# Kernel optimization log

Measured on AMD Instinct MI355X. Metric: run time of the kernel, lower is better.

## Reference

```python
import jax, jax.numpy as jnp
import numpy as np

B, S, D = 64, 14, 2048   # batch, enc_image_size, encoder_dim
A, H, E = 512, 512, 512  # attention_dim, lstm_size, embedding_size
V, L = 10000, 20         # vocab_size, max caption length (T = L-1 decode steps)


def setup_inputs() -> dict:
    key = jax.random.key(0)
    ks = jax.random.split(key, 24)
    p = lambda k, shape: jax.random.normal(k, shape, jnp.float32) * 0.02
    features = jax.random.normal(ks[0], (B, S, S, D), jnp.float32)
    captions = jax.random.randint(ks[1], (B, L), 0, V)
    # sorted descending lengths in [2, L], max forced to L so T_dec = L-1
    lengths = jnp.sort(jax.random.randint(ks[2], (B,), 2, L + 1))[::-1]
    lengths = lengths.at[0].set(L)
    return {
        'features': features, 'captions': captions, 'lengths': lengths,
        'emb': p(ks[3], (V, E)),
        'W_ih': p(ks[4], (4 * H, D + E)), 'b_ih': p(ks[5], (4 * H,)),
        'W_hh': p(ks[6], (4 * H, H)), 'b_hh': p(ks[7], (4 * H,)),
        'h_fc_w': p(ks[8], (H, D)), 'h_fc_b': p(ks[9], (H,)),
        'c_fc_w': p(ks[10], (H, D)), 'c_fc_b': p(ks[11], (H,)),
        'f_beta_w': p(ks[12], (D, H)), 'f_beta_b': p(ks[13], (D,)),
        'cls_w': p(ks[14], (V, H)), 'cls_b': p(ks[15], (V,)),
        'enc_w': p(ks[16], (A, D)), 'enc_b': p(ks[17], (A,)),
        'dec_w': p(ks[18], (A, H)), 'dec_b': p(ks[19], (A,)),
        'att_w': p(ks[20], (1, A)), 'att_b': p(ks[21], (1,)),
    }


def reference(features, captions, lengths, emb, W_ih, b_ih, W_hh, b_hh,
              h_fc_w, h_fc_b, c_fc_w, c_fc_b, f_beta_w, f_beta_b,
              cls_w, cls_b, enc_w, enc_b, dec_w, dec_b, att_w, att_b):
    feats = features.reshape(features.shape[0], -1, features.shape[-1])  # (B,P,D)
    emb_seq = emb[captions]                                              # (B,L,E)
    mean_f = feats.mean(axis=1)
    h = mean_f @ h_fc_w.T + h_fc_b
    c = mean_f @ c_fc_w.T + c_fc_b
    dec_len = lengths - 1
    T = captions.shape[1] - 1
    # attention encoder projection is time-invariant: hoist out of the loop
    att1 = jnp.einsum('bpd,ad->bpa', feats, enc_w) + enc_b               # (B,P,A)

    def step(carry, xs):
        h, c = carry
        x_emb, t = xs
        att2 = h @ dec_w.T + dec_b                                       # (B,A)
        e = jnp.einsum('bpa,a->bp', jax.nn.relu(att1 + att2[:, None, :]), att_w[0]) + att_b[0]
        alpha = jax.nn.softmax(e, axis=1)                                # (B,P)
        awe = jnp.einsum('bp,bpd->bd', alpha, feats)
        gate = jax.nn.sigmoid(h @ f_beta_w.T + f_beta_b)
        awe = gate * awe
        x = jnp.concatenate([x_emb, awe], axis=1)                        # (B,E+D)
        gates = x @ W_ih.T + b_ih + h @ W_hh.T + b_hh                    # torch gate order i,f,g,o
        i, f, g, o = jnp.split(gates, 4, axis=1)
        c2 = jax.nn.sigmoid(f) * c + jax.nn.sigmoid(i) * jnp.tanh(g)
        h2 = jax.nn.sigmoid(o) * jnp.tanh(c2)
        y = h2 @ cls_w.T + cls_b                                         # dropout = eval identity
        active = (t < dec_len)[:, None]
        return (h2, c2), (jnp.where(active, y, 0.0), jnp.where(active, alpha, 0.0))

    xs = (jnp.swapaxes(emb_seq[:, :T], 0, 1), jnp.arange(T))
    (_, _), (y_pred, alphas) = jax.lax.scan(step, (h, c), xs)
    return jnp.swapaxes(y_pred, 0, 1), jnp.swapaxes(alphas, 0, 1)
```

## Files before the change

### kernel.cpp

```cpp
#include <hip/hip_runtime.h>
#include <math.h>

typedef __attribute__((ext_vector_type(8))) short bf16x8;
typedef __attribute__((ext_vector_type(8))) unsigned short u16x8;
typedef __attribute__((ext_vector_type(4))) float f32x4;

#define NB 64
#define NP 196
#define ND 2048
#define NA 512
#define NH 512
#define NE 512
#define NV 10000
#define NT 19
#define NROW (NB*NP)
#define NVP 10112
#define MROW 1280
#define NHP 4608

__device__ __forceinline__ unsigned short f2bu(float f){
    unsigned int u; __builtin_memcpy(&u, &f, 4);
    u = (u + 0x7FFFu + ((u >> 16) & 1u)) >> 16;
    return (unsigned short)u;
}
__device__ __forceinline__ float b2f(unsigned short s){
    unsigned int u = ((unsigned int)s) << 16;
    float f; __builtin_memcpy(&f, &u, 4); return f;
}
__device__ __forceinline__ float sigm(float x){ return 1.f/(1.f + __expf(-x)); }

__device__ __forceinline__ void gll16(const void* g, void* l){
    __builtin_amdgcn_global_load_lds(
        (const __attribute__((address_space(1))) void*)g,
        (__attribute__((address_space(3))) void*)l, 16, 0, 0);
}


__global__ void k_prep(const float4* __restrict__ enc_w, const float4* __restrict__ dec_w,
                       const float4* __restrict__ f_beta_w, const float4* __restrict__ W_ih,
                       const float4* __restrict__ W_hh, const float4* __restrict__ h_fc_w,
                       const float4* __restrict__ c_fc_w, const float4* __restrict__ cls_w,
                       ushort4* __restrict__ encwb, ushort4* __restrict__ whp,
                       ushort4* __restrict__ wgates, ushort4* __restrict__ wembb,
                       ushort4* __restrict__ whc, ushort4* __restrict__ clswb,
                       ushort4* __restrict__ hsb_pad){
    const int n0 = NA*ND/4;
    const int n1 = NHP*512/4;
    const int n2 = 2048*2048/4;
    const int n3 = 2048*512/4;
    const int n4 = 1024*2048/4;
    const int n5 = NVP*NH/4;
    const int n6 = 64*512/4;
    const int total = n0+n1+n2+n3+n4+n5+n6;
    int stride = gridDim.x*blockDim.x;
    for (int i = blockIdx.x*blockDim.x + threadIdx.x; i < total; i += stride){
        int idx = i;
        float4 v; ushort4 o;
        if (idx < n0){
            v = enc_w[idx];
            o.x = f2bu(v.x); o.y = f2bu(v.y); o.z = f2bu(v.z); o.w = f2bu(v.w);
            encwb[idx] = o; continue;
        }
        idx -= n0;
        if (idx < n1){
            if (idx < 512*512/4) v = dec_w[idx];
            else if (idx < 2560*512/4) v = f_beta_w[idx - 512*512/4];
            else v = W_hh[idx - 2560*512/4];
            o.x = f2bu(v.x); o.y = f2bu(v.y); o.z = f2bu(v.z); o.w = f2bu(v.w);
            whp[idx] = o; continue;
        }
        idx -= n1;
        if (idx < n2){
            int j = idx >> 9, kk4 = idx & 511;
            v = W_ih[(size_t)j*640 + 128 + kk4];
            o.x = f2bu(v.x); o.y = f2bu(v.y); o.z = f2bu(v.z); o.w = f2bu(v.w);
            wgates[idx] = o; continue;
        }
        idx -= n2;
        if (idx < n3){
            int j = idx >> 7, kk4 = idx & 127;
            v = W_ih[(size_t)j*640 + kk4];
            o.x = f2bu(v.x); o.y = f2bu(v.y); o.z = f2bu(v.z); o.w = f2bu(v.w);
            wembb[idx] = o; continue;
        }
        idx -= n3;
        if (idx < n4){
            v = (idx < 512*2048/4) ? h_fc_w[idx] : c_fc_w[idx - 512*2048/4];
            o.x = f2bu(v.x); o.y = f2bu(v.y); o.z = f2bu(v.z); o.w = f2bu(v.w);
            whc[idx] = o; continue;
        }
        idx -= n4;
        if (idx < n5){
            if (idx < NV*NH/4){
                v = cls_w[idx];
                o.x = f2bu(v.x); o.y = f2bu(v.y); o.z = f2bu(v.z); o.w = f2bu(v.w);
            } else { o.x = 0; o.y = 0; o.z = 0; o.w = 0; }
            clswb[idx] = o; continue;
        }
        idx -= n5;
        o.x = 0; o.y = 0; o.z = 0; o.w = 0;
        hsb_pad[idx] = o;
    }
}

__global__ void k_cm(const float* __restrict__ feats,
                     unsigned short* __restrict__ fbf,
                     unsigned short* __restrict__ meanbf){
    __shared__ float4 msum[256];
    int dc = blockIdx.x;
    int b  = blockIdx.y;
    int tid = threadIdx.x;
    int c4 = tid & 63;
    int rq = tid >> 6;
    int D0 = dc*256;
    float4 acc = {0.f,0.f,0.f,0.f};
    for (int p = rq; p < NP; p += 4){
        float4 v = *(const float4*)(feats + ((size_t)(b*NP + p))*ND + D0 + c4*4);
        acc.x += v.x; acc.y += v.y; acc.z += v.z; acc.w += v.w;
        ushort4 u4;
        u4.x = f2bu(v.x); u4.y = f2bu(v.y); u4.z = f2bu(v.z); u4.w = f2bu(v.w);
        *(ushort4*)(fbf + ((size_t)(b*NP + p))*ND + D0 + c4*4) = u4;
    }
    msum[tid] = acc;
    __syncthreads();
    if (tid < 64){
        float4 s0 = msum[tid], s1 = msum[tid+64], s2 = msum[tid+128], s3 = msum[tid+192];
        float4 tot = { (s0.x+s1.x)+(s2.x+s3.x), (s0.y+s1.y)+(s2.y+s3.y),
                       (s0.z+s1.z)+(s2.z+s3.z), (s0.w+s1.w)+(s2.w+s3.w) };
        ushort4 o;
        o.x = f2bu(tot.x*(1.f/196.f)); o.y = f2bu(tot.y*(1.f/196.f));
        o.z = f2bu(tot.z*(1.f/196.f)); o.w = f2bu(tot.w*(1.f/196.f));
        *(ushort4*)(meanbf + (size_t)b*ND + D0 + tid*4) = o;
    }
}

__global__ void k_embg(const float* __restrict__ emb, const int* __restrict__ captions,
                       unsigned short* __restrict__ embcat){
    int blk = blockIdx.x, tid = threadIdx.x;
    int r = blk*4 + (tid >> 6);
    int cg = tid & 63;
    u16x8 o;
    #pragma unroll
    for (int k = 0; k < 8; k++) o[k] = 0;
    if (r < NT*64){
        int t = r >> 6, b = r & 63;
        int tok = captions[b*20 + t];
        const float* e = emb + (size_t)tok*NE + cg*8;
        float4 v0 = *(const float4*)e;
        float4 v1 = *(const float4*)(e + 4);
        o[0] = f2bu(v0.x); o[1] = f2bu(v0.y); o[2] = f2bu(v0.z); o[3] = f2bu(v0.w);
        o[4] = f2bu(v1.x); o[5] = f2bu(v1.y); o[6] = f2bu(v1.z); o[7] = f2bu(v1.w);
    }
    *(u16x8*)(embcat + (size_t)r*NE + cg*8) = o;
}

__global__ void k_hc0m(const unsigned short* __restrict__ meanbf,
                       const unsigned short* __restrict__ whc,
                       const float* __restrict__ h_fc_b, const float* __restrict__ c_fc_b,
                       unsigned short* __restrict__ hbf, float* __restrict__ cst){
    int tid = threadIdx.x;
    int w = tid >> 6, l = tid & 63;
    int nt = blockIdx.x;
    int row = 16*w + (l & 15);
    int col = nt*16 + (l & 15);
    int kg = (l >> 4) * 8;
    f32x4 acc = {};
    for (int k0 = 0; k0 < ND; k0 += 32){
        bf16x8 af = *(const bf16x8*)(meanbf + (size_t)row*ND + k0 + kg);
        bf16x8 bv = *(const bf16x8*)(whc + (size_t)col*ND + k0 + kg);
        acc = __builtin_amdgcn_mfma_f32_16x16x32_bf16(af, bv, acc, 0, 0, 0);
    }
    int r0 = 16*w + (l >> 4)*4;
    #pragma unroll
    for (int r = 0; r < 4; r++){
        int b = r0 + r;
        if (col < 512) hbf[b*NH + col] = f2bu(acc[r] + h_fc_b[col]);
        else           cst[b*NH + (col - 512)] = acc[r] + c_fc_b[col - 512];
    }
}

template<int K>
__device__ __forceinline__ void gemm128(const unsigned short* __restrict__ A,
                                        const unsigned short* __restrict__ B,
                                        int brow, int bcol, f32x4 acc[4][4]){
    __shared__ unsigned short As[128*32];
    __shared__ unsigned short Bs[128*32];
    int tid = threadIdx.x;
    int w = tid >> 6, l = tid & 63;
    int wr = (w >> 1) * 64, wc = (w & 1) * 64;
    int lr = l & 15, kg = (l >> 4) * 8;
    const unsigned short* ga0 = A + (size_t)(brow + (tid >> 2))*K + (tid & 3)*8;
    const unsigned short* gb0 = B + (size_t)(bcol + (tid >> 2))*K + (tid & 3)*8;
    for (int k0 = 0; k0 < K; k0 += 32){
        __syncthreads();
        gll16(ga0 + k0,                As + w*512);
        gll16(ga0 + (size_t)64*K + k0, As + 2048 + w*512);
        gll16(gb0 + k0,                Bs + w*512);
        gll16(gb0 + (size_t)64*K + k0, Bs + 2048 + w*512);
        __syncthreads();
        bf16x8 af[4], bfr[4];
        #pragma unroll
        for (int mi = 0; mi < 4; mi++)
            af[mi] = *(const bf16x8*)(As + (wr + mi*16 + lr)*32 + kg);
        #pragma unroll
        for (int ni = 0; ni < 4; ni++)
            bfr[ni] = *(const bf16x8*)(Bs + (wc + ni*16 + lr)*32 + kg);
        #pragma unroll
        for (int ni = 0; ni < 4; ni++){
            #pragma unroll
            for (int mi = 0; mi < 4; mi++)
                acc[mi][ni] = __builtin_amdgcn_mfma_f32_16x16x32_bf16(af[mi], bfr[ni], acc[mi][ni], 0, 0, 0);
        }
    }
}

__global__ void k_gemm_att1(const unsigned short* __restrict__ fbf,
                            const unsigned short* __restrict__ encw,
                            const float* __restrict__ enc_b,
                            unsigned short* __restrict__ att1){
    f32x4 acc[4][4] = {};
    int brow = blockIdx.x*128, bcol = blockIdx.y*128;
    gemm128<ND>(fbf, encw, brow, bcol, acc);
    int w = threadIdx.x >> 6, l = threadIdx.x & 63;
    int wr = (w >> 1) * 64, wc = (w & 1) * 64;
    int r0 = brow + wr + (l >> 4)*4;
    int c0 = bcol + wc + (l & 15);
    #pragma unroll
    for (int ni = 0; ni < 4; ni++){
        int col = c0 + ni*16;
        float eb = enc_b[col];
        #pragma unroll
        for (int mi = 0; mi < 4; mi++){
            #pragma unroll
            for (int r = 0; r < 4; r++)
                att1[(size_t)(r0 + mi*16 + r)*NA + col] = f2bu(acc[mi][ni][r] + eb);
        }
    }
}

__global__ void k_gemb(const unsigned short* __restrict__ embcat,
                       const unsigned short* __restrict__ wembb,
                       const float* __restrict__ b_ih, const float* __restrict__ b_hh,
                       float* __restrict__ gemb){
    f32x4 acc[4][4] = {};
    int brow = blockIdx.x*128, bcol = blockIdx.y*128;
    gemm128<NE>(embcat, wembb, brow, bcol, acc);
    int w = threadIdx.x >> 6, l = threadIdx.x & 63;
    int wr = (w >> 1) * 64, wc = (w & 1) * 64;
    int r0 = brow + wr + (l >> 4)*4;
    int c0 = bcol + wc + (l & 15);
    #pragma unroll
    for (int ni = 0; ni < 4; ni++){
        int col = c0 + ni*16;
        float bias = b_ih[col] + b_hh[col];
        #pragma unroll
        for (int mi = 0; mi < 4; mi++){
            #pragma unroll
            for (int r = 0; r < 4; r++)
                gemb[(size_t)(r0 + mi*16 + r)*2048 + col] = acc[mi][ni][r] + bias;
        }
    }
}

__global__ void k_gemm_cls(const unsigned short* __restrict__ hsb,
                           const unsigned short* __restrict__ clsw,
                           const float* __restrict__ cls_b,
                           const int* __restrict__ lengths,
                           float* __restrict__ yout){
    f32x4 acc[4][4] = {};
    int brow = blockIdx.x*128, bcol = blockIdx.y*128;
    gemm128<NH>(hsb, clsw, brow, bcol, acc);
    int w = threadIdx.x >> 6, l = threadIdx.x & 63;
    int wr = (w >> 1) * 64, wc = (w & 1) * 64;
    int r0 = brow + wr + (l >> 4)*4;
    int c0 = bcol + wc + (l & 15);
    #pragma unroll
    for (int ni = 0; ni < 4; ni++){
        int col = c0 + ni*16;
        if (col >= NV) continue;
        float cb = cls_b[col];
        #pragma unroll
        for (int mi = 0; mi < 4; mi++){
            #pragma unroll
            for (int r = 0; r < 4; r++){
                int grow = r0 + mi*16 + r;
                if (grow >= NT*64) continue;
                int t = grow >> 6, bb = grow & 63;
                int active = t < (lengths[bb] - 1);
                yout[((size_t)bb*NT + t)*NV + col] = active ? (acc[mi][ni][r] + cb) : 0.f;
            }
        }
    }
}


__global__ void k_lstm(const float* __restrict__ part, const float* __restrict__ gemb,
                       const float* __restrict__ hp,
                       float* __restrict__ cst, unsigned short* __restrict__ hbf,
                       unsigned short* __restrict__ hsb, int t){
    int idx = blockIdx.x*256 + threadIdx.x;
    int b = idx >> 9, j = idx & 511;
    const float* ge = gemb + ((size_t)(t - 1)*64 + b)*2048;
    const float* hh = hp + (size_t)b*NHP + 2560;
    float gi = ge[j]        + hh[j];
    float gf = ge[512 + j]  + hh[512 + j];
    float gg = ge[1024 + j] + hh[1024 + j];
    float go = ge[1536 + j] + hh[1536 + j];
    #pragma unroll
    for (int s = 0; s < 8; s++){
        const float* pb = part + (size_t)(s*64 + b)*2048;
        gi += pb[j]; gf += pb[512 + j]; gg += pb[1024 + j]; go += pb[1536 + j];
    }
    float c = cst[b*NH + j];
    float c2 = sigm(gf)*c + sigm(gi)*tanhf(gg);
    float h2 = sigm(go)*tanhf(c2);
    cst[b*NH + j] = c2;
    unsigned short u = f2bu(h2);
    hbf[b*NH + j] = u;
    hsb[((size_t)(t - 1)*64 + b)*NH + j] = u;
}

__global__ void k_hall(const unsigned short* __restrict__ hbf,
                       const unsigned short* __restrict__ whp,
                       const float* __restrict__ dec_b, const float* __restrict__ f_beta_b,
                       float* __restrict__ hp){
    int w = threadIdx.x >> 6, l = threadIdx.x & 63;
    int nt = blockIdx.x;
    int row = 16*w + (l & 15);
    int col = nt*16 + (l & 15);
    int kg = (l >> 4) * 8;
    f32x4 acc = {};
    for (int k0 = 0; k0 < NH; k0 += 32){
        bf16x8 af = *(const bf16x8*)(hbf + row*NH + k0 + kg);
        bf16x8 bv = *(const bf16x8*)(whp + (size_t)col*NH + k0 + kg);
        acc = __builtin_amdgcn_mfma_f32_16x16x32_bf16(af, bv, acc, 0, 0, 0);
    }
    int r0 = 16*w + (l >> 4)*4;
    float bias = (col < 512) ? dec_b[col] : ((col < 2560) ? f_beta_b[col - 512] : 0.f);
    #pragma unroll
    for (int r = 0; r < 4; r++)
        hp[(size_t)(r0 + r)*NHP + col] = acc[r] + bias;
}

__global__ void k_e(const unsigned short* __restrict__ att1,
                    const float* __restrict__ hp,
                    const float* __restrict__ att_w, const float* __restrict__ att_b,
                    float* __restrict__ ews){
    __shared__ float at2[NA];
    __shared__ float aw[NA];
    int b = blockIdx.x >> 2, pc = blockIdx.x & 3;
    int tid = threadIdx.x;
    for (int j = tid; j < NA; j += 256){
        at2[j] = hp[(size_t)b*NHP + j];
        aw[j]  = att_w[j];
    }
    __syncthreads();
    int pl = tid >> 2, q = tid & 3;
    if (pl < 49){
        int p = pc*49 + pl;
        const unsigned short* arow = att1 + ((size_t)(b*NP + p))*NA + q*128;
        float s = 0.f;
        for (int a0 = 0; a0 < 128; a0 += 8){
            bf16x8 v = *(const bf16x8*)(arow + a0);
            #pragma unroll
            for (int e = 0; e < 8; e++){
                int ai = q*128 + a0 + e;
                float x = b2f((unsigned short)v[e]) + at2[ai];
                s += fmaxf(x, 0.f) * aw[ai];
            }
        }
        s += __shfl_xor(s, 1);
        s += __shfl_xor(s, 2);
        if (q == 0) ews[b*NP + p] = s + att_b[0];
    }
}

__global__ void k_awe(const float* __restrict__ ews, const unsigned short* __restrict__ fbf,
                      const float* __restrict__ hp, const int* __restrict__ lengths,
                      unsigned short* __restrict__ xg, float* __restrict__ alphas, int t){
    __shared__ float al[NP];
    __shared__ float red[256];
    int dc = blockIdx.x;
    int b  = blockIdx.y;
    int tid = threadIdx.x;
    float v = (tid < NP) ? ews[b*NP + tid] : -1e30f;
    red[tid] = v; __syncthreads();
    for (int s = 128; s > 0; s >>= 1){ if (tid < s) red[tid] = fmaxf(red[tid], red[tid+s]); __syncthreads(); }
    float m = red[0]; __syncthreads();
    float ev = (tid < NP) ? __expf(v - m) : 0.f;
    red[tid] = ev; __syncthreads();
    for (int s = 128; s > 0; s >>= 1){ if (tid < s) red[tid] += red[tid+s]; __syncthreads(); }
    float inv = 1.f / red[0];
    if (tid < NP) al[tid] = ev * inv;
    __syncthreads();
    if (dc == 0 && tid < NP){
        int active = t < (lengths[b] - 1);
        alphas[((size_t)b*NT + t)*NP + tid] = active ? al[tid] : 0.f;
    }
    int d = dc*256 + tid;
    const unsigned short* fb = fbf + (size_t)(b*NP)*ND + d;
    float a0 = 0.f, a1 = 0.f, a2 = 0.f, a3 = 0.f;
    for (int p = 0; p < 196; p += 4){
        a0 += al[p]     * b2f(fb[(size_t)p*ND]);
        a1 += al[p + 1] * b2f(fb[(size_t)(p + 1)*ND]);
        a2 += al[p + 2] * b2f(fb[(size_t)(p + 2)*ND]);
        a3 += al[p + 3] * b2f(fb[(size_t)(p + 3)*ND]);
    }
    float accv = (a0 + a1) + (a2 + a3);
    float g = sigm(hp[(size_t)b*NHP + 512 + d]);
    xg[b*2048 + d] = f2bu(g * accv);
}

__global__ void k_gates(const unsigned short* __restrict__ xg,
                        const unsigned short* __restrict__ wgates,
                        float* __restrict__ part){
    int nt = blockIdx.x;
    int s  = blockIdx.y;
    int w = threadIdx.x >> 6, l = threadIdx.x & 63;
    int row = 16*w + (l & 15);
    int col = nt*16 + (l & 15);
    int kg = (l >> 4) * 8;
    const unsigned short* arow = xg + row*2048 + s*256;
    const unsigned short* brow = wgates + (size_t)col*2048 + s*256;
    f32x4 acc = {};
    for (int k0 = 0; k0 < 256; k0 += 32){
        bf16x8 af = *(const bf16x8*)(arow + k0 + kg);
        bf16x8 bv = *(const bf16x8*)(brow + k0 + kg);
        acc = __builtin_amdgcn_mfma_f32_16x16x32_bf16(af, bv, acc, 0, 0, 0);
    }
    int r0 = 16*w + (l >> 4)*4;
    #pragma unroll
    for (int r = 0; r < 4; r++)
        part[(size_t)(s*64 + r0 + r)*2048 + col] = acc[r];
}

__global__ void k_lstm_fin(const float* __restrict__ part, const float* __restrict__ gemb,
                           const float* __restrict__ hp,
                           const float* __restrict__ cst, unsigned short* __restrict__ hsb){
    int idx = blockIdx.x*256 + threadIdx.x;
    int b = idx >> 9, j = idx & 511;
    const float* ge = gemb + ((size_t)(NT - 1)*64 + b)*2048;
    const float* hh = hp + (size_t)b*NHP + 2560;
    float gi = ge[j]        + hh[j];
    float gf = ge[512 + j]  + hh[512 + j];
    float gg = ge[1024 + j] + hh[1024 + j];
    float go = ge[1536 + j] + hh[1536 + j];
    #pragma unroll
    for (int s = 0; s < 8; s++){
        const float* pb = part + (size_t)(s*64 + b)*2048;
        gi += pb[j]; gf += pb[512 + j]; gg += pb[1024 + j]; go += pb[1536 + j];
    }
    float c = cst[b*NH + j];
    float c2 = sigm(gf)*c + sigm(gi)*tanhf(gg);
    float h2 = sigm(go)*tanhf(c2);
    hsb[((size_t)(NT - 1)*64 + b)*NH + j] = f2bu(h2);
}


extern "C" void kernel_launch(void* const* d_in, const int* in_sizes, int n_in,
                              void* d_out, int out_size, void* d_ws, size_t ws_size,
                              hipStream_t stream){
    const float* features = (const float*)d_in[0];
    const int*   captions = (const int*)d_in[1];
    const int*   lengths  = (const int*)d_in[2];
    const float* emb      = (const float*)d_in[3];
    const float* W_ih     = (const float*)d_in[4];
    const float* b_ih     = (const float*)d_in[5];
    const float* W_hh     = (const float*)d_in[6];
    const float* b_hh     = (const float*)d_in[7];
    const float* h_fc_w   = (const float*)d_in[8];
    const float* h_fc_b   = (const float*)d_in[9];
    const float* c_fc_w   = (const float*)d_in[10];
    const float* c_fc_b   = (const float*)d_in[11];
    const float* f_beta_w = (const float*)d_in[12];
    const float* f_beta_b = (const float*)d_in[13];
    const float* cls_w    = (const float*)d_in[14];
    const float* cls_b    = (const float*)d_in[15];
    const float* enc_w    = (const float*)d_in[16];
    const float* enc_b    = (const float*)d_in[17];
    const float* dec_w    = (const float*)d_in[18];
    const float* dec_b    = (const float*)d_in[19];
    const float* att_w    = (const float*)d_in[20];
    const float* att_b    = (const float*)d_in[21];

    char* w = (char*)d_ws;
    size_t off = 0;
    auto alloc = [&](size_t bytes)->char*{
        char* p = w + off;
        off += (bytes + 255) & ~(size_t)255;
        return p;
    };
    unsigned short* fbf    = (unsigned short*)alloc((size_t)NROW*ND*2);
    unsigned short* att1   = (unsigned short*)alloc((size_t)NROW*NA*2);
    unsigned short* encwb  = (unsigned short*)alloc((size_t)NA*ND*2);
    unsigned short* whp    = (unsigned short*)alloc((size_t)NHP*NH*2);
    unsigned short* wgates = (unsigned short*)alloc((size_t)2048*2048*2);
    unsigned short* wembb  = (unsigned short*)alloc((size_t)2048*NE*2);
    unsigned short* whc    = (unsigned short*)alloc((size_t)1024*ND*2);
    unsigned short* clswb  = (unsigned short*)alloc((size_t)NVP*NH*2);
    unsigned short* embcat = (unsigned short*)alloc((size_t)MROW*NE*2);
    unsigned short* hsb    = (unsigned short*)alloc((size_t)MROW*NH*2);
    unsigned short* hbf    = (unsigned short*)alloc((size_t)64*NH*2);
    unsigned short* xg     = (unsigned short*)alloc((size_t)64*2048*2);
    unsigned short* meanbf = (unsigned short*)alloc((size_t)64*ND*2);
    float* gemb  = (float*)alloc((size_t)MROW*2048*4);
    float* cst   = (float*)alloc((size_t)64*NH*4);
    float* hp    = (float*)alloc((size_t)64*NHP*4);
    float* ews   = (float*)alloc((size_t)64*NP*4);
    float* part  = (float*)alloc((size_t)8*64*2048*4);

    float* yout = (float*)d_out;
    float* alphas_out = yout + (size_t)NB*NT*NV;

    k_cm<<<dim3(8, 64), 256, 0, stream>>>(features, fbf, meanbf);
    k_prep<<<2048, 256, 0, stream>>>((const float4*)enc_w, (const float4*)dec_w,
                                     (const float4*)f_beta_w, (const float4*)W_ih,
                                     (const float4*)W_hh, (const float4*)h_fc_w,
                                     (const float4*)c_fc_w, (const float4*)cls_w,
                                     (ushort4*)encwb, (ushort4*)whp, (ushort4*)wgates,
                                     (ushort4*)wembb, (ushort4*)whc, (ushort4*)clswb,
                                     (ushort4*)(hsb + (size_t)NT*64*NH));
    k_embg<<<320, 256, 0, stream>>>(emb, captions, embcat);
    k_hc0m<<<64, 256, 0, stream>>>(meanbf, whc, h_fc_b, c_fc_b, hbf, cst);
    k_gemm_att1<<<dim3(98, 4), 256, 0, stream>>>(fbf, encwb, enc_b, att1);
    k_gemb<<<dim3(10, 16), 256, 0, stream>>>(embcat, wembb, b_ih, b_hh, gemb);

    for (int t = 0; t < NT; t++){
        if (t > 0)
            k_lstm<<<128, 256, 0, stream>>>(part, gemb, hp, cst, hbf, hsb, t);
        k_hall<<<288, 256, 0, stream>>>(hbf, whp, dec_b, f_beta_b, hp);
        k_e<<<256, 256, 0, stream>>>(att1, hp, att_w, att_b, ews);
        k_awe<<<dim3(8, 64), 256, 0, stream>>>(ews, fbf, hp, lengths, xg, alphas_out, t);
        k_gates<<<dim3(128, 8), 256, 0, stream>>>(xg, wgates, part);
    }
    k_lstm_fin<<<128, 256, 0, stream>>>(part, gemb, hp, cst, hsb);
    k_gemm_cls<<<dim3(10, 79), 256, 0, stream>>>(hsb, clswb, cls_b, lengths, yout);
}
```

Baseline: 1.054 ms.

## Fuse attention score with weighted sum, and gate GEMM with LSTM cell update

The per-step loop drops from five kernels to three. Attention scores and softmax are now computed inside the weighted-sum kernel, with each block redoing the full score pass for its batch row. The gate GEMM now does split-K reduction through shared memory within a 1024-thread block, with an interleaved column layout so one wave holds all four gates and can apply the LSTM cell update directly. This removes the ews and part global round-trips and several launches per step. The cost is redundant score computation (4x per batch row) and fewer blocks (256 and 128), which risks lower parallelism.

```diff
diff --git a/kernel.cpp b/kernel.cpp
--- a/kernel.cpp
+++ b/kernel.cpp
@@ -294,32 +294,6 @@
 }
 
 
-__global__ void k_lstm(const float* __restrict__ part, const float* __restrict__ gemb,
-                       const float* __restrict__ hp,
-                       float* __restrict__ cst, unsigned short* __restrict__ hbf,
-                       unsigned short* __restrict__ hsb, int t){
-    int idx = blockIdx.x*256 + threadIdx.x;
-    int b = idx >> 9, j = idx & 511;
-    const float* ge = gemb + ((size_t)(t - 1)*64 + b)*2048;
-    const float* hh = hp + (size_t)b*NHP + 2560;
-    float gi = ge[j]        + hh[j];
-    float gf = ge[512 + j]  + hh[512 + j];
-    float gg = ge[1024 + j] + hh[1024 + j];
-    float go = ge[1536 + j] + hh[1536 + j];
-    #pragma unroll
-    for (int s = 0; s < 8; s++){
-        const float* pb = part + (size_t)(s*64 + b)*2048;
-        gi += pb[j]; gf += pb[512 + j]; gg += pb[1024 + j]; go += pb[1536 + j];
-    }
-    float c = cst[b*NH + j];
-    float c2 = sigm(gf)*c + sigm(gi)*tanhf(gg);
-    float h2 = sigm(go)*tanhf(c2);
-    cst[b*NH + j] = c2;
-    unsigned short u = f2bu(h2);
-    hbf[b*NH + j] = u;
-    hsb[((size_t)(t - 1)*64 + b)*NH + j] = u;
-}
-
 __global__ void k_hall(const unsigned short* __restrict__ hbf,
                        const unsigned short* __restrict__ whp,
                        const float* __restrict__ dec_b, const float* __restrict__ f_beta_b,
@@ -342,13 +316,18 @@
         hp[(size_t)(r0 + r)*NHP + col] = acc[r] + bias;
 }
 
-__global__ void k_e(const unsigned short* __restrict__ att1,
-                    const float* __restrict__ hp,
-                    const float* __restrict__ att_w, const float* __restrict__ att_b,
-                    float* __restrict__ ews){
+__global__ void k_eawe(const unsigned short* __restrict__ att1,
+                       const float* __restrict__ hp,
+                       const unsigned short* __restrict__ fbf,
+                       const float* __restrict__ att_w, const float* __restrict__ att_b,
+                       const int* __restrict__ lengths,
+                       unsigned short* __restrict__ xg, float* __restrict__ alphas, int t){
     __shared__ float at2[NA];
     __shared__ float aw[NA];
-    int b = blockIdx.x >> 2, pc = blockIdx.x & 3;
+    __shared__ float sc[200];
+    __shared__ float red[256];
+    int dc = blockIdx.x;
+    int b  = blockIdx.y;
     int tid = threadIdx.x;
     for (int j = tid; j < NA; j += 256){
         at2[j] = hp[(size_t)b*NHP + j];
@@ -356,104 +335,114 @@
     }
     __syncthreads();
     int pl = tid >> 2, q = tid & 3;
-    if (pl < 49){
-        int p = pc*49 + pl;
-        const unsigned short* arow = att1 + ((size_t)(b*NP + p))*NA + q*128;
-        float s = 0.f;
-        for (int a0 = 0; a0 < 128; a0 += 8){
-            bf16x8 v = *(const bf16x8*)(arow + a0);
-            #pragma unroll
-            for (int e = 0; e < 8; e++){
-                int ai = q*128 + a0 + e;
-                float x = b2f((unsigned short)v[e]) + at2[ai];
-                s += fmaxf(x, 0.f) * aw[ai];
+    float ab = att_b[0];
+    #pragma unroll
+    for (int pc = 0; pc < 4; pc++){
+        if (pl < 49){
+            int p = pc*49 + pl;
+            const unsigned short* arow = att1 + ((size_t)(b*NP + p))*NA + q*128;
+            float s = 0.f;
+            for (int a0 = 0; a0 < 128; a0 += 8){
+                bf16x8 v = *(const bf16x8*)(arow + a0);
+                #pragma unroll
+                for (int e = 0; e < 8; e++){
+                    int ai = q*128 + a0 + e;
+                    float x = b2f((unsigned short)v[e]) + at2[ai];
+                    s += fmaxf(x, 0.f) * aw[ai];
+                }
             }
-        }
-        s += __shfl_xor(s, 1);
-        s += __shfl_xor(s, 2);
-        if (q == 0) ews[b*NP + p] = s + att_b[0];
-    }
-}
-
-__global__ void k_awe(const float* __restrict__ ews, const unsigned short* __restrict__ fbf,
-                      const float* __restrict__ hp, const int* __restrict__ lengths,
-                      unsigned short* __restrict__ xg, float* __restrict__ alphas, int t){
-    __shared__ float al[NP];
-    __shared__ float red[256];
-    int dc = blockIdx.x;
-    int b  = blockIdx.y;
-    int tid = threadIdx.x;
-    float v = (tid < NP) ? ews[b*NP + tid] : -1e30f;
+            s += __shfl_xor(s, 1);
+            s += __shfl_xor(s, 2);
+            if (q == 0) sc[p] = s + ab;
+        }
+    }
+    __syncthreads();
+    float v = (tid < NP) ? sc[tid] : -1e30f;
     red[tid] = v; __syncthreads();
-    for (int s = 128; s > 0; s >>= 1){ if (tid < s) red[tid] = fmaxf(red[tid], red[tid+s]); __syncthreads(); }
+    for (int st = 128; st > 0; st >>= 1){ if (tid < st) red[tid] = fmaxf(red[tid], red[tid+st]); __syncthreads(); }
     float m = red[0]; __syncthreads();
     float ev = (tid < NP) ? __expf(v - m) : 0.f;
     red[tid] = ev; __syncthreads();
-    for (int s = 128; s > 0; s >>= 1){ if (tid < s) red[tid] += red[tid+s]; __syncthreads(); }
+    for (int st = 128; st > 0; st >>= 1){ if (tid < st) red[tid] += red[tid+st]; __syncthreads(); }
     float inv = 1.f / red[0];
-    if (tid < NP) al[tid] = ev * inv;
+    __syncthreads();
+    if (tid < NP) sc[tid] = ev * inv;
     __syncthreads();
     if (dc == 0 && tid < NP){
         int active = t < (lengths[b] - 1);
-        alphas[((size_t)b*NT + t)*NP + tid] = active ? al[tid] : 0.f;
-    }
-    int d = dc*256 + tid;
-    const unsigned short* fb = fbf + (size_t)(b*NP)*ND + d;
+        alphas[((size_t)b*NT + t)*NP + tid] = active ? sc[tid] : 0.f;
+    }
+    int d0 = dc*512 + tid;
+    const unsigned short* fb = fbf + (size_t)(b*NP)*ND;
     float a0 = 0.f, a1 = 0.f, a2 = 0.f, a3 = 0.f;
+    float b0 = 0.f, b1 = 0.f, b2 = 0.f, b3 = 0.f;
     for (int p = 0; p < 196; p += 4){
-        a0 += al[p]     * b2f(fb[(size_t)p*ND]);
-        a1 += al[p + 1] * b2f(fb[(size_t)(p + 1)*ND]);
-        a2 += al[p + 2] * b2f(fb[(size_t)(p + 2)*ND]);
-        a3 += al[p + 3] * b2f(fb[(size_t)(p + 3)*ND]);
-    }
-    float accv = (a0 + a1) + (a2 + a3);
-    float g = sigm(hp[(size_t)b*NHP + 512 + d]);
-    xg[b*2048 + d] = f2bu(g * accv);
-}
-
-__global__ void k_gates(const unsigned short* __restrict__ xg,
-                        const unsigned short* __restrict__ wgates,
-                        float* __restrict__ part){
+        const unsigned short* f0 = fb + (size_t)p*ND + d0;
+        float l0 = sc[p], l1 = sc[p+1], l2 = sc[p+2], l3 = sc[p+3];
+        a0 += l0 * b2f(f0[0]);        a1 += l1 * b2f(f0[ND]);
+        a2 += l2 * b2f(f0[2*ND]);     a3 += l3 * b2f(f0[3*ND]);
+        b0 += l0 * b2f(f0[256]);      b1 += l1 * b2f(f0[ND + 256]);
+        b2 += l2 * b2f(f0[2*ND + 256]); b3 += l3 * b2f(f0[3*ND + 256]);
+    }
+    float awe0 = (a0 + a1) + (a2 + a3);
+    float awe1 = (b0 + b1) + (b2 + b3);
+    float g0 = sigm(hp[(size_t)b*NHP + 512 + d0]);
+    float g1 = sigm(hp[(size_t)b*NHP + 512 + d0 + 256]);
+    xg[b*2048 + d0]       = f2bu(g0 * awe0);
+    xg[b*2048 + d0 + 256] = f2bu(g1 * awe1);
+}
+
+__global__ void __launch_bounds__(1024) k_gla(
+        const unsigned short* __restrict__ xg,
+        const unsigned short* __restrict__ wgates,
+        const float* __restrict__ gemb, const float* __restrict__ hp,
+        float* __restrict__ cst, unsigned short* __restrict__ hbf,
+        unsigned short* __restrict__ hsb, int t){
+    __shared__ f32x4 lred[3][4][64];
+    int tid = threadIdx.x;
+    int w = tid >> 6, l = tid & 63;
+    int mi = w & 3, ks = w >> 2;
     int nt = blockIdx.x;
-    int s  = blockIdx.y;
-    int w = threadIdx.x >> 6, l = threadIdx.x & 63;
-    int row = 16*w + (l & 15);
-    int col = nt*16 + (l & 15);
+    int cl = l & 15;
+    int j  = nt*4 + (cl >> 2);
+    int g  = cl & 3;
     int kg = (l >> 4) * 8;
-    const unsigned short* arow = xg + row*2048 + s*256;
-    const unsigned short* brow = wgates + (size_t)col*2048 + s*256;
+    const unsigned short* arow = xg + (size_t)(mi*16 + cl)*2048 + ks*512;
+    const unsigned short* brow = wgates + ((size_t)g*512 + j)*2048 + ks*512;
     f32x4 acc = {};
-    for (int k0 = 0; k0 < 256; k0 += 32){
+    for (int k0 = 0; k0 < 512; k0 += 32){
         bf16x8 af = *(const bf16x8*)(arow + k0 + kg);
         bf16x8 bv = *(const bf16x8*)(brow + k0 + kg);
         acc = __builtin_amdgcn_mfma_f32_16x16x32_bf16(af, bv, acc, 0, 0, 0);
     }
-    int r0 = 16*w + (l >> 4)*4;
-    #pragma unroll
-    for (int r = 0; r < 4; r++)
-        part[(size_t)(s*64 + r0 + r)*2048 + col] = acc[r];
-}
-
-__global__ void k_lstm_fin(const float* __restrict__ part, const float* __restrict__ gemb,
-                           const float* __restrict__ hp,
-                           const float* __restrict__ cst, unsigned short* __restrict__ hsb){
-    int idx = blockIdx.x*256 + threadIdx.x;
-    int b = idx >> 9, j = idx & 511;
-    const float* ge = gemb + ((size_t)(NT - 1)*64 + b)*2048;
-    const float* hh = hp + (size_t)b*NHP + 2560;
-    float gi = ge[j]        + hh[j];
-    float gf = ge[512 + j]  + hh[512 + j];
-    float gg = ge[1024 + j] + hh[1024 + j];
-    float go = ge[1536 + j] + hh[1536 + j];
-    #pragma unroll
-    for (int s = 0; s < 8; s++){
-        const float* pb = part + (size_t)(s*64 + b)*2048;
-        gi += pb[j]; gf += pb[512 + j]; gg += pb[1024 + j]; go += pb[1536 + j];
-    }
-    float c = cst[b*NH + j];
-    float c2 = sigm(gf)*c + sigm(gi)*tanhf(gg);
-    float h2 = sigm(go)*tanhf(c2);
-    hsb[((size_t)(NT - 1)*64 + b)*NH + j] = f2bu(h2);
+    if (ks > 0) lred[ks - 1][mi][l] = acc;
+    __syncthreads();
+    if (ks == 0){
+        f32x4 s1 = lred[0][mi][l], s2 = lred[1][mi][l], s3 = lred[2][mi][l];
+        #pragma unroll
+        for (int r = 0; r < 4; r++) acc[r] += (s1[r] + s2[r]) + s3[r];
+        const float* ge = gemb + (size_t)t*64*2048;
+        int gcol = g*512 + j;
+        #pragma unroll
+        for (int rr = 0; rr < 4; rr++){
+            int row = mi*16 + (l >> 4)*4 + rr;
+            float gval = acc[rr] + ge[(size_t)row*2048 + gcol]
+                       + hp[(size_t)row*NHP + 2560 + gcol];
+            float vi = __shfl(gval, (l & ~3) + 0);
+            float vf = __shfl(gval, (l & ~3) + 1);
+            float vg = __shfl(gval, (l & ~3) + 2);
+            float vo = __shfl(gval, (l & ~3) + 3);
+            if ((l & 3) == 0){
+                float cp = cst[row*NH + j];
+                float c2 = sigm(vf)*cp + sigm(vi)*tanhf(vg);
+                float h2 = sigm(vo)*tanhf(c2);
+                cst[row*NH + j] = c2;
+                unsigned short u = f2bu(h2);
+                hbf[row*NH + j] = u;
+                hsb[((size_t)t*64 + row)*NH + j] = u;
+            }
+        }
+    }
 }
 
 
@@ -506,8 +495,6 @@
     float* gemb  = (float*)alloc((size_t)MROW*2048*4);
     float* cst   = (float*)alloc((size_t)64*NH*4);
     float* hp    = (float*)alloc((size_t)64*NHP*4);
-    float* ews   = (float*)alloc((size_t)64*NP*4);
-    float* part  = (float*)alloc((size_t)8*64*2048*4);
 
     float* yout = (float*)d_out;
     float* alphas_out = yout + (size_t)NB*NT*NV;
@@ -526,13 +513,10 @@
     k_gemb<<<dim3(10, 16), 256, 0, stream>>>(embcat, wembb, b_ih, b_hh, gemb);
 
     for (int t = 0; t < NT; t++){
-        if (t > 0)
-            k_lstm<<<128, 256, 0, stream>>>(part, gemb, hp, cst, hbf, hsb, t);
         k_hall<<<288, 256, 0, stream>>>(hbf, whp, dec_b, f_beta_b, hp);
-        k_e<<<256, 256, 0, stream>>>(att1, hp, att_w, att_b, ews);
-        k_awe<<<dim3(8, 64), 256, 0, stream>>>(ews, fbf, hp, lengths, xg, alphas_out, t);
-        k_gates<<<dim3(128, 8), 256, 0, stream>>>(xg, wgates, part);
-    }
-    k_lstm_fin<<<128, 256, 0, stream>>>(part, gemb, hp, cst, hsb);
+        k_eawe<<<dim3(4, 64), 256, 0, stream>>>(att1, hp, fbf, att_w, att_b,
+                                                lengths, xg, alphas_out, t);
+        k_gla<<<128, 1024, 0, stream>>>(xg, wgates, gemb, hp, cst, hbf, hsb, t);
+    }
     k_gemm_cls<<<dim3(10, 79), 256, 0, stream>>>(hsb, clswb, cls_b, lengths, yout);
 }
```

Result: slower. 1.540 ms (+46.1%).

## Move W_hh·h projection off critical path into gates kernel; widen mean kernel

Applied to the files above, without the earlier changes.

The k_hall launch now computes only the attention and gate projections (2560 columns). The recurrent W_hh·h part (columns 2560+) moves into an extra ninth y-slice of k_gates, so it runs alongside the gates GEMM instead of before the attention kernels on the serial per-step chain. k_cm also goes from 256 to 1024 threads per block, splitting the feature sum over more rows, with a 16-way shared-memory reduction. The cost is a larger k_gates grid and a bigger reduction step, but k_hall, which sits on the critical path of every decode step, gets lighter.

```diff
diff --git a/kernel.cpp b/kernel.cpp
--- a/kernel.cpp
+++ b/kernel.cpp
@@ -103,10 +103,10 @@
     }
 }
 
-__global__ void k_cm(const float* __restrict__ feats,
-                     unsigned short* __restrict__ fbf,
-                     unsigned short* __restrict__ meanbf){
-    __shared__ float4 msum[256];
+__global__ void __launch_bounds__(1024) k_cm(const float* __restrict__ feats,
+                                             unsigned short* __restrict__ fbf,
+                                             unsigned short* __restrict__ meanbf){
+    __shared__ float4 msum[1024];
     int dc = blockIdx.x;
     int b  = blockIdx.y;
     int tid = threadIdx.x;
@@ -114,7 +114,7 @@
     int rq = tid >> 6;
     int D0 = dc*256;
     float4 acc = {0.f,0.f,0.f,0.f};
-    for (int p = rq; p < NP; p += 4){
+    for (int p = rq; p < NP; p += 16){
         float4 v = *(const float4*)(feats + ((size_t)(b*NP + p))*ND + D0 + c4*4);
         acc.x += v.x; acc.y += v.y; acc.z += v.z; acc.w += v.w;
         ushort4 u4;
@@ -124,9 +124,12 @@
     msum[tid] = acc;
     __syncthreads();
     if (tid < 64){
-        float4 s0 = msum[tid], s1 = msum[tid+64], s2 = msum[tid+128], s3 = msum[tid+192];
-        float4 tot = { (s0.x+s1.x)+(s2.x+s3.x), (s0.y+s1.y)+(s2.y+s3.y),
-                       (s0.z+s1.z)+(s2.z+s3.z), (s0.w+s1.w)+(s2.w+s3.w) };
+        float4 tot = {0.f,0.f,0.f,0.f};
+        #pragma unroll
+        for (int k = 0; k < 16; k++){
+            float4 s = msum[tid + 64*k];
+            tot.x += s.x; tot.y += s.y; tot.z += s.z; tot.w += s.w;
+        }
         ushort4 o;
         o.x = f2bu(tot.x*(1.f/196.f)); o.y = f2bu(tot.y*(1.f/196.f));
         o.z = f2bu(tot.z*(1.f/196.f)); o.w = f2bu(tot.w*(1.f/196.f));
@@ -336,7 +339,7 @@
         acc = __builtin_amdgcn_mfma_f32_16x16x32_bf16(af, bv, acc, 0, 0, 0);
     }
     int r0 = 16*w + (l >> 4)*4;
-    float bias = (col < 512) ? dec_b[col] : ((col < 2560) ? f_beta_b[col - 512] : 0.f);
+    float bias = (col < 512) ? dec_b[col] : f_beta_b[col - 512];
     #pragma unroll
     for (int r = 0; r < 4; r++)
         hp[(size_t)(r0 + r)*NHP + col] = acc[r] + bias;
@@ -412,14 +415,29 @@
 }
 
 __global__ void k_gates(const unsigned short* __restrict__ xg,
+                        const unsigned short* __restrict__ hbf,
+                        const unsigned short* __restrict__ whp,
                         const unsigned short* __restrict__ wgates,
-                        float* __restrict__ part){
+                        float* __restrict__ part, float* __restrict__ hp){
     int nt = blockIdx.x;
     int s  = blockIdx.y;
     int w = threadIdx.x >> 6, l = threadIdx.x & 63;
     int row = 16*w + (l & 15);
     int col = nt*16 + (l & 15);
     int kg = (l >> 4) * 8;
+    if (s == 8){
+        f32x4 acc = {};
+        for (int k0 = 0; k0 < NH; k0 += 32){
+            bf16x8 af = *(const bf16x8*)(hbf + row*NH + k0 + kg);
+            bf16x8 bv = *(const bf16x8*)(whp + (size_t)(2560 + col)*NH + k0 + kg);
+            acc = __builtin_amdgcn_mfma_f32_16x16x32_bf16(af, bv, acc, 0, 0, 0);
+        }
+        int r0 = 16*w + (l >> 4)*4;
+        #pragma unroll
+        for (int r = 0; r < 4; r++)
+            hp[(size_t)(r0 + r)*NHP + 2560 + col] = acc[r];
+        return;
+    }
     const unsigned short* arow = xg + row*2048 + s*256;
     const unsigned short* brow = wgates + (size_t)col*2048 + s*256;
     f32x4 acc = {};
@@ -512,7 +530,7 @@
     float* yout = (float*)d_out;
     float* alphas_out = yout + (size_t)NB*NT*NV;
 
-    k_cm<<<dim3(8, 64), 256, 0, stream>>>(features, fbf, meanbf);
+    k_cm<<<dim3(8, 64), 1024, 0, stream>>>(features, fbf, meanbf);
     k_prep<<<2048, 256, 0, stream>>>((const float4*)enc_w, (const float4*)dec_w,
                                      (const float4*)f_beta_w, (const float4*)W_ih,
                                      (const float4*)W_hh, (const float4*)h_fc_w,
@@ -528,10 +546,10 @@
     for (int t = 0; t < NT; t++){
         if (t > 0)
             k_lstm<<<128, 256, 0, stream>>>(part, gemb, hp, cst, hbf, hsb, t);
-        k_hall<<<288, 256, 0, stream>>>(hbf, whp, dec_b, f_beta_b, hp);
+        k_hall<<<160, 256, 0, stream>>>(hbf, whp, dec_b, f_beta_b, hp);
         k_e<<<256, 256, 0, stream>>>(att1, hp, att_w, att_b, ews);
         k_awe<<<dim3(8, 64), 256, 0, stream>>>(ews, fbf, hp, lengths, xg, alphas_out, t);
-        k_gates<<<dim3(128, 8), 256, 0, stream>>>(xg, wgates, part);
+        k_gates<<<dim3(128, 9), 256, 0, stream>>>(xg, hbf, whp, wgates, part, hp);
     }
     k_lstm_fin<<<128, 256, 0, stream>>>(part, gemb, hp, cst, hsb);
     k_gemm_cls<<<dim3(10, 79), 256, 0, stream>>>(hsb, clswb, cls_b, lengths, yout);
```

Result: no change. 1.034 ms (-1.9%).
